# Kernel optimization log

Hardware: AMD Instinct MI355X
Metric: run time of the kernel (lower is better)

The kernel has to match this reference:

```python
import jax, jax.numpy as jnp
import numpy as np

F_IN, HID, F_OUT = 8, 64, 8
R, C = 256, 4096
NUM_SETS, N_IND, M = 3, 4096, 4096


def setup_inputs() -> dict:
    key = jax.random.key(0)
    k0, k1, k2 = jax.random.split(key, 3)
    input_tensor = jax.random.normal(k0, (F_IN, R, C), dtype=jnp.float32)
    w1 = jax.random.normal(k1, (HID, 3 * F_IN), dtype=jnp.float32) * 0.1
    b1 = jnp.zeros((HID,), jnp.float32)
    w2 = jax.random.normal(k2, (F_OUT, HID), dtype=jnp.float32) * 0.1
    b2 = jnp.zeros((F_OUT,), jnp.float32)
    rng = np.random.default_rng(0)
    def make_ind():
        # col0: permutation of [0, N_IND) (duplicate-free scatter-set destinations)
        # col1: random source column in [0, C)
        col0 = np.stack([rng.permutation(N_IND) for _ in range(NUM_SETS)])
        col1 = rng.integers(0, C, size=(NUM_SETS, N_IND))
        return jnp.asarray(np.stack([col0, col1], axis=-1), jnp.int32)
    ind0, ind1, ind2 = make_ind(), make_ind(), make_ind()
    mix_ind = jnp.asarray(rng.integers(0, N_IND, size=(NUM_SETS, 3, M)), jnp.int32)
    return {"input_tensor": input_tensor, "w1": w1, "b1": b1, "w2": w2, "b2": b2,
            "ind0": ind0, "ind1": ind1, "ind2": ind2, "mix_ind": mix_ind}


def reference(input_tensor, w1, b1, w2, b2, ind0, ind1, ind2, mix_ind):
    # Output for row r depends only on input row r, so we process all R at once
    # (the original chunk loop over R is pure tiling).
    F_in, Rr, Cc = input_tensor.shape
    F_out = w2.shape[0]
    num_sets = ind0.shape[0]

    def project(ind, mi):
        # res[..., ind[:,0]] = input[..., ind[:,1]]; then take slots mi -> [F_in, R, M]
        n = ind.shape[0]
        res = jnp.zeros((F_in, Rr, n), input_tensor.dtype)
        res = res.at[..., ind[:, 0]].set(input_tensor[..., ind[:, 1]])
        return res[..., mi]

    out_rcf = jnp.zeros((Rr, Cc, F_out), input_tensor.dtype)  # zeros = include_self baseline
    for s in range(num_sets):
        c1 = project(ind0[s], mix_ind[s, 0])
        c2 = project(ind1[s], mix_ind[s, 1])
        c3 = project(ind2[s], mix_ind[s, 2])
        c = jnp.concatenate([c1, c2, c3], axis=0)          # [3F_in, R, M]
        c_flat = c.transpose(1, 2, 0).reshape(-1, 3 * F_in)  # [R*M, 3F_in]
        a1 = jax.nn.relu(c_flat @ w1.T + b1)                 # [R*M, HID]
        d = (a1 @ w2.T + b2).reshape(Rr, -1, F_out)          # [R, M, F_out]
        for i, ind in enumerate((ind0[s], ind1[s], ind2[s])):
            idx = ind[:, 1][mix_ind[s, i]]                   # [M] target columns in C
            out_rcf = out_rcf.at[:, idx, :].max(d)           # amax scatter, include_self
    return out_rcf.transpose(2, 0, 1)                        # [F_out, R, C]
```

## Files before the change

### kernel.cpp

```cpp
#include <hip/hip_runtime.h>
#include <cstdint>

#define F_IN   8
#define HID    64
#define F_OUTD 8
#define RDIM   256
#define CDIM   4096
#define NSETS  3
#define NIND   4096
#define MDIM   4096
#define CAP    16
#define MAXL   48
#define GC     16
#define MPW    4

using short8 = __attribute__((ext_vector_type(8))) short;
using f32x4  = __attribute__((ext_vector_type(4))) float;

__device__ inline unsigned int cvtpk(float a, float b) {
    unsigned int r;
    asm("v_cvt_pk_bf16_f32 %0, %1, %2" : "=v"(r) : "v"(a), "v"(b));
    return r;
}
__device__ inline unsigned int pkmaxu(unsigned int a, unsigned int b) {
    unsigned int r;
    asm("v_pk_max_u16 %0, %1, %2" : "=v"(r) : "v"(a), "v"(b));
    return r;
}

__global__ __launch_bounds__(256)
void prep_in(const float* __restrict__ in, unsigned short* __restrict__ out) {
    const int PADH = 264;
    __shared__ unsigned short tile[32 * PADH];
    int c0 = blockIdx.x * 32, r0 = blockIdx.y * 32;
    int t = threadIdx.x;
    int tx = t & 31, ty = t >> 5;
#pragma unroll
    for (int f = 0; f < 8; f += 2)
#pragma unroll
        for (int rr = 0; rr < 4; rr++) {
            int r = ty + rr * 8;
            float v0 = in[((size_t)f * RDIM + (r0 + r)) * CDIM + c0 + tx];
            float v1 = in[((size_t)(f + 1) * RDIM + (r0 + r)) * CDIM + c0 + tx];
            *(unsigned int*)&tile[tx * PADH + r * 8 + f] = cvtpk(v0, v1);
        }
    __syncthreads();
    int r = t & 31, cl = t >> 5;
#pragma unroll
    for (int cc = 0; cc < 4; cc++) {
        int c = cc * 8 + cl;
        uint4 v = *(const uint4*)&tile[c * PADH + r * 8];
        *(uint4*)(out + (((size_t)(c0 + c) * RDIM) + (r0 + r)) * 8) = v;
    }
}

__global__ void build_inv(const int* __restrict__ ind0, const int* __restrict__ ind1,
                          const int* __restrict__ ind2,
                          const float* __restrict__ w1, const float* __restrict__ w2,
                          int* __restrict__ inv, int* __restrict__ cnt,
                          unsigned short* __restrict__ w1bf, unsigned short* __restrict__ w2bf) {
    int k  = blockIdx.x * 256 + threadIdx.x;
    int si = blockIdx.y;
    int s_ = si / 3, i_ = si % 3;
    const int* ind = (i_ == 0 ? ind0 : (i_ == 1 ? ind1 : ind2)) + (size_t)s_ * NIND * 2;
    int c0 = ind[2 * k];
    inv[(size_t)si * NIND + c0] = k;
    cnt[si * CDIM + k] = 0;
    if (blockIdx.x == 0 && blockIdx.y == 0) {
        int t = threadIdx.x;
        for (int i = t; i < 64 * 32; i += 256) {
            int j = i >> 5, kk = i & 31;
            w1bf[i] = (kk < 24) ? (unsigned short)(cvtpk(w1[j * 24 + kk], 0.f) & 0xffff) : 0;
        }
        for (int i = t; i < 16 * 64; i += 256) {
            int f = i >> 6, kg = i & 63;
            int hi = kg >> 5, q = (kg >> 3) & 3, e = kg & 7;
            int j = (hi << 5) + ((e >> 2) << 4) + (q << 2) + (e & 3);
            w2bf[i] = (f < 8) ? (unsigned short)(cvtpk(w2[f * 64 + j], 0.f) & 0xffff) : 0;
        }
    }
}

__global__ void build_buckets(const int* __restrict__ ind0, const int* __restrict__ ind1,
                              const int* __restrict__ ind2, const int* __restrict__ mix,
                              int* __restrict__ cnt, int* __restrict__ list) {
    int m  = blockIdx.x * 256 + threadIdx.x;
    int si = blockIdx.y;
    int s_ = si / 3, i_ = si % 3;
    const int* ind = (i_ == 0 ? ind0 : (i_ == 1 ? ind1 : ind2)) + (size_t)s_ * NIND * 2;
    int mi = mix[(size_t)si * MDIM + m];
    int c  = ind[2 * mi + 1];
    int slot = atomicAdd(&cnt[si * CDIM + c], 1);
    if (slot < CAP) list[((size_t)si * CDIM + c) * CAP + slot] = m;
}

__global__ __launch_bounds__(256, 2)
void mlp_store(const unsigned short* __restrict__ inT2,
               const unsigned short* __restrict__ w1bf,
               const unsigned short* __restrict__ w2bf,
               const float* __restrict__ b1, const float* __restrict__ b2,
               const int* __restrict__ ind0, const int* __restrict__ ind1,
               const int* __restrict__ ind2, const int* __restrict__ mix,
               const int* __restrict__ inv,
               unsigned short* __restrict__ dbuf) {
    int t    = threadIdx.x;
    int wave = t >> 6, lane = t & 63;
    int lo = lane & 15, q = lane >> 4;

    int wid  = blockIdx.x * 4 + wave;
    int mgrp = wid & 1023;
    int half = (wid >> 10) & 1;
    int s_   = wid >> 11;
    int m0   = mgrp * MPW;

    short8 A1[4], A2[2];
#pragma unroll
    for (int tt = 0; tt < 4; tt++)
        A1[tt] = *(const short8*)(w1bf + ((16 * tt + lo) << 5) + (q << 3));
#pragma unroll
    for (int kk = 0; kk < 2; kk++)
        A2[kk] = *(const short8*)(w2bf + (lo << 6) + (kk << 5) + (q << 3));

    f32x4 bbv[4];
#pragma unroll
    for (int tt = 0; tt < 4; tt++)
#pragma unroll
        for (int rg = 0; rg < 4; rg++)
            bbv[tt][rg] = b1[16 * tt + 4 * q + rg];
    f32x4 b2f;
#pragma unroll
    for (int rg = 0; rg < 4; rg++) {
        int f = 4 * q + rg;
        b2f[rg] = (f < 8) ? b2[f] : 0.f;
    }

    int gq[MPW] = {0, 0, 0, 0};
    if (q < 3) {
        int si = s_ * 3 + q;
        const int* indq = (q == 0 ? ind0 : (q == 1 ? ind1 : ind2)) + (size_t)s_ * NIND * 2;
        int mi[MPW], kk[MPW];
#pragma unroll
        for (int u = 0; u < MPW; u++) mi[u] = mix[(size_t)si * MDIM + m0 + u];
#pragma unroll
        for (int u = 0; u < MPW; u++) kk[u] = inv[(size_t)si * NIND + mi[u]];
#pragma unroll
        for (int u = 0; u < MPW; u++) gq[u] = indq[2 * kk[u] + 1];
    }
    const unsigned short* srcs[MPW];
#pragma unroll
    for (int u = 0; u < MPW; u++)
        srcs[u] = inT2 + ((size_t)gq[u] * RDIM + half * 128 + lo) * 8;

    unsigned short* dst = dbuf + (size_t)(s_ * MDIM + m0) * 2048 + half * 1024 + lo * 8 + q * 4;

    union U { unsigned int u[4]; short8 s; };
    const short8 zero8 = {0, 0, 0, 0, 0, 0, 0, 0};

    short8 Bcur = zero8;
    if (q < 3) Bcur = *(const short8*)srcs[0];
#pragma unroll
    for (int it = 0; it < MPW * 8; it++) {
        const int u = it >> 3, j = it & 7;
        short8 Bnext = Bcur;
        if (it < MPW * 8 - 1 && q < 3)
            Bnext = *(const short8*)(srcs[(it + 1) >> 3] + ((it + 1) & 7) * 128);

        f32x4 a0 = __builtin_amdgcn_mfma_f32_16x16x32_bf16(A1[0], Bcur, bbv[0], 0, 0, 0);
        f32x4 a1 = __builtin_amdgcn_mfma_f32_16x16x32_bf16(A1[1], Bcur, bbv[1], 0, 0, 0);
        f32x4 a2 = __builtin_amdgcn_mfma_f32_16x16x32_bf16(A1[2], Bcur, bbv[2], 0, 0, 0);
        f32x4 a3 = __builtin_amdgcn_mfma_f32_16x16x32_bf16(A1[3], Bcur, bbv[3], 0, 0, 0);

        U ba, bb;
        ba.u[0] = cvtpk(fmaxf(a0[0], 0.f), fmaxf(a0[1], 0.f));
        ba.u[1] = cvtpk(fmaxf(a0[2], 0.f), fmaxf(a0[3], 0.f));
        ba.u[2] = cvtpk(fmaxf(a1[0], 0.f), fmaxf(a1[1], 0.f));
        ba.u[3] = cvtpk(fmaxf(a1[2], 0.f), fmaxf(a1[3], 0.f));
        bb.u[0] = cvtpk(fmaxf(a2[0], 0.f), fmaxf(a2[1], 0.f));
        bb.u[1] = cvtpk(fmaxf(a2[2], 0.f), fmaxf(a2[3], 0.f));
        bb.u[2] = cvtpk(fmaxf(a3[0], 0.f), fmaxf(a3[1], 0.f));
        bb.u[3] = cvtpk(fmaxf(a3[2], 0.f), fmaxf(a3[3], 0.f));

        f32x4 o = __builtin_amdgcn_mfma_f32_16x16x32_bf16(A2[0], ba.s, b2f, 0, 0, 0);
        o = __builtin_amdgcn_mfma_f32_16x16x32_bf16(A2[1], bb.s, o, 0, 0, 0);

        if (q < 2) {
            uint2 ov;
            ov.x = cvtpk(fmaxf(o[0], 0.f), fmaxf(o[1], 0.f));
            ov.y = cvtpk(fmaxf(o[2], 0.f), fmaxf(o[3], 0.f));
            *(uint2*)(dst + (size_t)u * 2048 + j * 128) = ov;
        }
        Bcur = Bnext;
    }
}

__global__ __launch_bounds__(256)
void gather_max_t(const unsigned short* __restrict__ dbuf, const int* __restrict__ cnt,
                  const int* __restrict__ list, float* __restrict__ out) {
    __shared__ float ldsT[8][16][20];
    __shared__ int   mlist[GC][MAXL];
    __shared__ int   mcnt[GC];
    int c0 = blockIdx.x * GC;
    int t  = threadIdx.x;
    int tc = t >> 4, tr = t & 15;
    int c  = c0 + tc;

    if (tr == 0) {
        int n = 0;
        for (int si = 0; si < 9; si++) {
            int s = si / 3;
            int k = cnt[si * CDIM + c]; if (k > CAP) k = CAP;
            const int* lp = list + ((size_t)si * CDIM + c) * CAP;
            for (int e = 0; e < k && n < MAXL; e++)
                mlist[tc][n++] = s * MDIM + lp[e];
        }
        mcnt[tc] = n;
    }
    __syncthreads();
    int n = mcnt[tc];

    uint4 acc[4];
#pragma unroll
    for (int p = 0; p < 4; p++) acc[p] = make_uint4(0u, 0u, 0u, 0u);

    int rbase = blockIdx.y * 64 + tr;
    for (int e = 0; e < n; e++) {
        int idx = mlist[tc][e];
        const unsigned short* bp = dbuf + ((size_t)idx * RDIM + rbase) * 8;
        uint4 v0 = *(const uint4*)(bp);
        uint4 v1 = *(const uint4*)(bp + 16 * 8);
        uint4 v2 = *(const uint4*)(bp + 32 * 8);
        uint4 v3 = *(const uint4*)(bp + 48 * 8);
        acc[0].x = pkmaxu(acc[0].x, v0.x); acc[0].y = pkmaxu(acc[0].y, v0.y);
        acc[0].z = pkmaxu(acc[0].z, v0.z); acc[0].w = pkmaxu(acc[0].w, v0.w);
        acc[1].x = pkmaxu(acc[1].x, v1.x); acc[1].y = pkmaxu(acc[1].y, v1.y);
        acc[1].z = pkmaxu(acc[1].z, v1.z); acc[1].w = pkmaxu(acc[1].w, v1.w);
        acc[2].x = pkmaxu(acc[2].x, v2.x); acc[2].y = pkmaxu(acc[2].y, v2.y);
        acc[2].z = pkmaxu(acc[2].z, v2.z); acc[2].w = pkmaxu(acc[2].w, v2.w);
        acc[3].x = pkmaxu(acc[3].x, v3.x); acc[3].y = pkmaxu(acc[3].y, v3.y);
        acc[3].z = pkmaxu(acc[3].z, v3.z); acc[3].w = pkmaxu(acc[3].w, v3.w);
    }

#pragma unroll
    for (int p = 0; p < 4; p++) {
        if (p) __syncthreads();
        ldsT[0][tr][tc] = __uint_as_float(acc[p].x << 16);
        ldsT[1][tr][tc] = __uint_as_float(acc[p].x & 0xffff0000u);
        ldsT[2][tr][tc] = __uint_as_float(acc[p].y << 16);
        ldsT[3][tr][tc] = __uint_as_float(acc[p].y & 0xffff0000u);
        ldsT[4][tr][tc] = __uint_as_float(acc[p].z << 16);
        ldsT[5][tr][tc] = __uint_as_float(acc[p].z & 0xffff0000u);
        ldsT[6][tr][tc] = __uint_as_float(acc[p].w << 16);
        ldsT[7][tr][tc] = __uint_as_float(acc[p].w & 0xffff0000u);
        __syncthreads();
#pragma unroll
        for (int k2 = 0; k2 < 2; k2++) {
            int idx2 = t * 2 + k2;
            int f = idx2 >> 6, rl = (idx2 >> 2) & 15, cq = idx2 & 3;
            *(float4*)&out[((size_t)f * RDIM + blockIdx.y * 64 + p * 16 + rl) * CDIM + c0 + cq * 4] =
                *(const float4*)&ldsT[f][rl][cq * 4];
        }
    }
}

extern "C" void kernel_launch(void* const* d_in, const int* in_sizes, int n_in,
                              void* d_out, int out_size, void* d_ws, size_t ws_size,
                              hipStream_t stream) {
    const float* input = (const float*)d_in[0];
    const float* w1    = (const float*)d_in[1];
    const float* b1    = (const float*)d_in[2];
    const float* w2    = (const float*)d_in[3];
    const float* b2    = (const float*)d_in[4];
    const int*   ind0  = (const int*)d_in[5];
    const int*   ind1  = (const int*)d_in[6];
    const int*   ind2  = (const int*)d_in[7];
    const int*   mix   = (const int*)d_in[8];

    const size_t MiB = 1ull << 20;
    char* ws = (char*)d_ws;
    unsigned short* inT2 = (unsigned short*)ws;
    unsigned short* dbuf = (unsigned short*)(ws + 16 * MiB);
    char* tail = ws + 64 * MiB;
    int* inv  = (int*)tail;
    int* cnt  = (int*)(tail + 147456);
    int* list = (int*)(tail + 2 * 147456);
    unsigned short* w1bf = (unsigned short*)(tail + 2 * 147456 + 9ull * CDIM * CAP * 4);
    unsigned short* w2bf = w1bf + 64 * 32;

    prep_in<<<dim3(CDIM / 32, RDIM / 32), 256, 0, stream>>>(input, inT2);
    build_inv<<<dim3(NIND / 256, 9), 256, 0, stream>>>(ind0, ind1, ind2, w1, w2,
                                                       inv, cnt, w1bf, w2bf);
    build_buckets<<<dim3(MDIM / 256, 9), 256, 0, stream>>>(ind0, ind1, ind2, mix, cnt, list);
    mlp_store<<<NSETS * 2 * (MDIM / MPW) / 4, 256, 0, stream>>>(inT2, w1bf, w2bf, b1, b2,
                                                                ind0, ind1, ind2, mix, inv, dbuf);
    gather_max_t<<<dim3(CDIM / GC, 4), 256, 0, stream>>>(dbuf, cnt, list, (float*)d_out);
}
```

Measured before the change: 94.04 us.

## Merge per-set bucket lists into one per-column list and prefetch gathers

Replaces the nine per-(set,index) bucket lists, each capped at 16, with a single merged per-column list capped at 64 and filled by one atomic counter. The gather kernel then loads the list cooperatively with 16 threads instead of one thread walking nine lists serially. The gather loop is also software-pipelined so the next row's loads are issued before the current max. This trades less setup latency for more contention on a single atomic per column, and it silently drops entries for any column with more than 64 hits.

```diff
diff --git a/kernel.cpp b/kernel.cpp
--- a/kernel.cpp
+++ b/kernel.cpp
@@ -9,8 +9,7 @@
 #define NSETS  3
 #define NIND   4096
 #define MDIM   4096
-#define CAP    16
-#define MAXL   48
+#define MAXL   64
 #define GC     16
 #define MPW    4
 
@@ -57,7 +56,7 @@
 __global__ void build_inv(const int* __restrict__ ind0, const int* __restrict__ ind1,
                           const int* __restrict__ ind2,
                           const float* __restrict__ w1, const float* __restrict__ w2,
-                          int* __restrict__ inv, int* __restrict__ cnt,
+                          int* __restrict__ inv, int* __restrict__ mergecnt,
                           unsigned short* __restrict__ w1bf, unsigned short* __restrict__ w2bf) {
     int k  = blockIdx.x * 256 + threadIdx.x;
     int si = blockIdx.y;
@@ -65,7 +64,7 @@
     const int* ind = (i_ == 0 ? ind0 : (i_ == 1 ? ind1 : ind2)) + (size_t)s_ * NIND * 2;
     int c0 = ind[2 * k];
     inv[(size_t)si * NIND + c0] = k;
-    cnt[si * CDIM + k] = 0;
+    if (si == 0) mergecnt[k] = 0;
     if (blockIdx.x == 0 && blockIdx.y == 0) {
         int t = threadIdx.x;
         for (int i = t; i < 64 * 32; i += 256) {
@@ -83,15 +82,15 @@
 
 __global__ void build_buckets(const int* __restrict__ ind0, const int* __restrict__ ind1,
                               const int* __restrict__ ind2, const int* __restrict__ mix,
-                              int* __restrict__ cnt, int* __restrict__ list) {
+                              int* __restrict__ mergecnt, int* __restrict__ mergelist) {
     int m  = blockIdx.x * 256 + threadIdx.x;
     int si = blockIdx.y;
     int s_ = si / 3, i_ = si % 3;
     const int* ind = (i_ == 0 ? ind0 : (i_ == 1 ? ind1 : ind2)) + (size_t)s_ * NIND * 2;
     int mi = mix[(size_t)si * MDIM + m];
     int c  = ind[2 * mi + 1];
-    int slot = atomicAdd(&cnt[si * CDIM + c], 1);
-    if (slot < CAP) list[((size_t)si * CDIM + c) * CAP + slot] = m;
+    int slot = atomicAdd(&mergecnt[c], 1);
+    if (slot < MAXL) mergelist[(size_t)c * MAXL + slot] = s_ * MDIM + m;
 }
 
 __global__ __launch_bounds__(256, 2)
@@ -194,50 +193,55 @@
 }
 
 __global__ __launch_bounds__(256)
-void gather_max_t(const unsigned short* __restrict__ dbuf, const int* __restrict__ cnt,
-                  const int* __restrict__ list, float* __restrict__ out) {
+void gather_max_t(const unsigned short* __restrict__ dbuf, const int* __restrict__ mergecnt,
+                  const int* __restrict__ mergelist, float* __restrict__ out) {
     __shared__ float ldsT[8][16][20];
     __shared__ int   mlist[GC][MAXL];
-    __shared__ int   mcnt[GC];
     int c0 = blockIdx.x * GC;
     int t  = threadIdx.x;
     int tc = t >> 4, tr = t & 15;
     int c  = c0 + tc;
 
-    if (tr == 0) {
-        int n = 0;
-        for (int si = 0; si < 9; si++) {
-            int s = si / 3;
-            int k = cnt[si * CDIM + c]; if (k > CAP) k = CAP;
-            const int* lp = list + ((size_t)si * CDIM + c) * CAP;
-            for (int e = 0; e < k && n < MAXL; e++)
-                mlist[tc][n++] = s * MDIM + lp[e];
-        }
-        mcnt[tc] = n;
-    }
+    int n = mergecnt[c]; if (n > MAXL) n = MAXL;
+    for (int e = tr; e < n; e += 16)
+        mlist[tc][e] = mergelist[(size_t)c * MAXL + e];
     __syncthreads();
-    int n = mcnt[tc];
 
     uint4 acc[4];
 #pragma unroll
     for (int p = 0; p < 4; p++) acc[p] = make_uint4(0u, 0u, 0u, 0u);
 
     int rbase = blockIdx.y * 64 + tr;
-    for (int e = 0; e < n; e++) {
-        int idx = mlist[tc][e];
-        const unsigned short* bp = dbuf + ((size_t)idx * RDIM + rbase) * 8;
-        uint4 v0 = *(const uint4*)(bp);
-        uint4 v1 = *(const uint4*)(bp + 16 * 8);
-        uint4 v2 = *(const uint4*)(bp + 32 * 8);
-        uint4 v3 = *(const uint4*)(bp + 48 * 8);
-        acc[0].x = pkmaxu(acc[0].x, v0.x); acc[0].y = pkmaxu(acc[0].y, v0.y);
-        acc[0].z = pkmaxu(acc[0].z, v0.z); acc[0].w = pkmaxu(acc[0].w, v0.w);
-        acc[1].x = pkmaxu(acc[1].x, v1.x); acc[1].y = pkmaxu(acc[1].y, v1.y);
-        acc[1].z = pkmaxu(acc[1].z, v1.z); acc[1].w = pkmaxu(acc[1].w, v1.w);
-        acc[2].x = pkmaxu(acc[2].x, v2.x); acc[2].y = pkmaxu(acc[2].y, v2.y);
-        acc[2].z = pkmaxu(acc[2].z, v2.z); acc[2].w = pkmaxu(acc[2].w, v2.w);
-        acc[3].x = pkmaxu(acc[3].x, v3.x); acc[3].y = pkmaxu(acc[3].y, v3.y);
-        acc[3].z = pkmaxu(acc[3].z, v3.z); acc[3].w = pkmaxu(acc[3].w, v3.w);
+    if (n > 0) {
+        const unsigned short* bp = dbuf + ((size_t)mlist[tc][0] * RDIM + rbase) * 8;
+        uint4 p0 = *(const uint4*)(bp);
+        uint4 p1 = *(const uint4*)(bp + 16 * 8);
+        uint4 p2 = *(const uint4*)(bp + 32 * 8);
+        uint4 p3 = *(const uint4*)(bp + 48 * 8);
+        for (int e = 1; e < n; e++) {
+            const unsigned short* bq = dbuf + ((size_t)mlist[tc][e] * RDIM + rbase) * 8;
+            uint4 q0 = *(const uint4*)(bq);
+            uint4 q1 = *(const uint4*)(bq + 16 * 8);
+            uint4 q2 = *(const uint4*)(bq + 32 * 8);
+            uint4 q3 = *(const uint4*)(bq + 48 * 8);
+            acc[0].x = pkmaxu(acc[0].x, p0.x); acc[0].y = pkmaxu(acc[0].y, p0.y);
+            acc[0].z = pkmaxu(acc[0].z, p0.z); acc[0].w = pkmaxu(acc[0].w, p0.w);
+            acc[1].x = pkmaxu(acc[1].x, p1.x); acc[1].y = pkmaxu(acc[1].y, p1.y);
+            acc[1].z = pkmaxu(acc[1].z, p1.z); acc[1].w = pkmaxu(acc[1].w, p1.w);
+            acc[2].x = pkmaxu(acc[2].x, p2.x); acc[2].y = pkmaxu(acc[2].y, p2.y);
+            acc[2].z = pkmaxu(acc[2].z, p2.z); acc[2].w = pkmaxu(acc[2].w, p2.w);
+            acc[3].x = pkmaxu(acc[3].x, p3.x); acc[3].y = pkmaxu(acc[3].y, p3.y);
+            acc[3].z = pkmaxu(acc[3].z, p3.z); acc[3].w = pkmaxu(acc[3].w, p3.w);
+            p0 = q0; p1 = q1; p2 = q2; p3 = q3;
+        }
+        acc[0].x = pkmaxu(acc[0].x, p0.x); acc[0].y = pkmaxu(acc[0].y, p0.y);
+        acc[0].z = pkmaxu(acc[0].z, p0.z); acc[0].w = pkmaxu(acc[0].w, p0.w);
+        acc[1].x = pkmaxu(acc[1].x, p1.x); acc[1].y = pkmaxu(acc[1].y, p1.y);
+        acc[1].z = pkmaxu(acc[1].z, p1.z); acc[1].w = pkmaxu(acc[1].w, p1.w);
+        acc[2].x = pkmaxu(acc[2].x, p2.x); acc[2].y = pkmaxu(acc[2].y, p2.y);
+        acc[2].z = pkmaxu(acc[2].z, p2.z); acc[2].w = pkmaxu(acc[2].w, p2.w);
+        acc[3].x = pkmaxu(acc[3].x, p3.x); acc[3].y = pkmaxu(acc[3].y, p3.y);
+        acc[3].z = pkmaxu(acc[3].z, p3.z); acc[3].w = pkmaxu(acc[3].w, p3.w);
     }
 
 #pragma unroll
@@ -280,17 +284,19 @@
     unsigned short* inT2 = (unsigned short*)ws;
     unsigned short* dbuf = (unsigned short*)(ws + 16 * MiB);
     char* tail = ws + 64 * MiB;
-    int* inv  = (int*)tail;
-    int* cnt  = (int*)(tail + 147456);
-    int* list = (int*)(tail + 2 * 147456);
-    unsigned short* w1bf = (unsigned short*)(tail + 2 * 147456 + 9ull * CDIM * CAP * 4);
+    int* inv       = (int*)tail;
+    int* mergecnt  = (int*)(tail + 147456);
+    int* mergelist = (int*)(tail + 147456 + 16384);
+    unsigned short* w1bf = (unsigned short*)(tail + 147456 + 16384 + (size_t)CDIM * MAXL * 4);
     unsigned short* w2bf = w1bf + 64 * 32;
 
     prep_in<<<dim3(CDIM / 32, RDIM / 32), 256, 0, stream>>>(input, inT2);
     build_inv<<<dim3(NIND / 256, 9), 256, 0, stream>>>(ind0, ind1, ind2, w1, w2,
-                                                       inv, cnt, w1bf, w2bf);
-    build_buckets<<<dim3(MDIM / 256, 9), 256, 0, stream>>>(ind0, ind1, ind2, mix, cnt, list);
+                                                       inv, mergecnt, w1bf, w2bf);
+    build_buckets<<<dim3(MDIM / 256, 9), 256, 0, stream>>>(ind0, ind1, ind2, mix,
+                                                           mergecnt, mergelist);
     mlp_store<<<NSETS * 2 * (MDIM / MPW) / 4, 256, 0, stream>>>(inT2, w1bf, w2bf, b1, b2,
                                                                 ind0, ind1, ind2, mix, inv, dbuf);
-    gather_max_t<<<dim3(CDIM / GC, 4), 256, 0, stream>>>(dbuf, cnt, list, (float*)d_out);
-}
+    gather_max_t<<<dim3(CDIM / GC, 4), 256, 0, stream>>>(dbuf, mergecnt, mergelist,
+                                                         (float*)d_out);
+}
```

Result: faster. 88.28 us (-6.1%).
